# Optimization experiments

Hardware: AMD Instinct MI355X
Metric: run time of the kernel (lower is better)

The kernel has to match this reference:

```python
import jax, jax.numpy as jnp
import numpy as np

EPS = 1e-5

def splice(x, offsets):
    # x: [B, F, T]; offsets already shifted so offsets[0] == 0.
    # Output channel order matches torch reshape(-1, C*F): y[b, f*C+c, t] = x[b, f, t+off[c]]
    w = offsets[-1]
    Tn = x.shape[2] - w
    y = jnp.stack([x[:, :, o:o + Tn] for o in offsets], axis=2)  # [B, F, C, Tn]
    B, F, C, _ = y.shape
    return y.reshape(B, F * C, Tn)

def conv1x1(x, w, b):
    # x: [B, Cin, T], w: [Cout, Cin], b: [Cout]
    return jnp.einsum('oc,bct->bot', w, x) + b[None, :, None]

def bn_ct(x, gamma=None, beta=None):
    # BatchNorm1d (training mode, biased var) over (batch, time) per channel
    m = x.mean(axis=(0, 2), keepdims=True)
    v = x.var(axis=(0, 2), keepdims=True)
    y = (x - m) * jax.lax.rsqrt(v + EPS)
    if gamma is not None:
        y = y * gamma[None, :, None] + beta[None, :, None]
    return y

def bn_c(x, gamma, beta):
    # BatchNorm1d on [B, C]
    m = x.mean(axis=0, keepdims=True)
    v = x.var(axis=0, keepdims=True)
    return (x - m) * jax.lax.rsqrt(v + EPS) * gamma[None, :] + beta[None, :]

def relu6(x):
    return jnp.clip(x, 0.0, 6.0)

def setup_inputs() -> dict:
    key = jax.random.key(0)
    ks = list(jax.random.split(key, 32))
    def rn(shape, scale=0.05):
        return jax.random.normal(ks.pop(), shape, dtype=jnp.float32) * scale
    inp = {
        'x': jax.random.normal(ks.pop(), (32, 2048, 20), dtype=jnp.float32),
        'h1_w': rn((512, 100)), 'h1_b': rn((512,)),
        'h2_w': rn((512, 1536)), 'h2_b': rn((512,)),
        'bn2_g': jnp.ones((512,), jnp.float32), 'bn2_b': jnp.zeros((512,), jnp.float32),
        'h3_w': rn((512, 1536)), 'h3_b': rn((512,)),
        'bn3_g': jnp.ones((512,), jnp.float32), 'bn3_b': jnp.zeros((512,), jnp.float32),
        'h4_w': rn((512, 512)), 'h4_b': rn((512,)),
        'bn4_g': jnp.ones((512,), jnp.float32), 'bn4_b': jnp.zeros((512,), jnp.float32),
        'h5_w': rn((1500, 512)), 'h5_b': rn((1500,)),
        'bn5_g': jnp.ones((1500,), jnp.float32), 'bn5_b': jnp.zeros((1500,), jnp.float32),
        'l1_w': rn((512, 3000)), 'l1_b': rn((512,)),
        'bn6_g': jnp.ones((512,), jnp.float32), 'bn6_b': jnp.zeros((512,), jnp.float32),
        'l2_w': rn((512, 512)), 'l2_b': rn((512,)),
        'bn7_g': jnp.ones((512,), jnp.float32), 'bn7_b': jnp.zeros((512,), jnp.float32),
    }
    return inp

def reference(x, h1_w, h1_b, h2_w, h2_b, bn2_g, bn2_b, h3_w, h3_b, bn3_g, bn3_b,
              h4_w, h4_b, bn4_g, bn4_b, h5_w, h5_b, bn5_g, bn5_b,
              l1_w, l1_b, bn6_g, bn6_b, l2_w, l2_b, bn7_g, bn7_b):
    o = jnp.transpose(x, (0, 2, 1))                     # [B, 20, T]
    o = splice(o, (0, 1, 2, 3, 4))                      # context [-2..2] -> [B, 100, T-4]
    o = bn_ct(jax.nn.relu(conv1x1(o, h1_w, h1_b)))      # bn1 affine=False
    o = splice(o, (0, 2, 4))                            # context [-2,0,2] -> [B, 1536, T-8]
    o = bn_ct(jax.nn.relu(conv1x1(o, h2_w, h2_b)), bn2_g, bn2_b)
    o = splice(o, (0, 3, 6))                            # context [-3,0,3] -> [B, 1536, T-14]
    o = bn_ct(jax.nn.relu(conv1x1(o, h3_w, h3_b)), bn3_g, bn3_b)
    o = bn_ct(relu6(conv1x1(o, h4_w, h4_b)), bn4_g, bn4_b)
    o = bn_ct(relu6(conv1x1(o, h5_w, h5_b)), bn5_g, bn5_b)  # [B, 1500, T']
    mean = o.mean(axis=-1)
    std = jnp.std(o, axis=-1, ddof=1)                   # torch.std is unbiased
    o = jnp.concatenate((mean, std), axis=1)            # [B, 3000]
    o = bn_c(relu6(o @ l1_w.T + l1_b), bn6_g, bn6_b)
    o = bn_c(relu6(o @ l2_w.T + l2_b), bn7_g, bn7_b)
    return o
```

## Files before the change

kernel.cpp:

```cpp
#include <hip/hip_runtime.h>
#include <cstdint>

#define EPSF 1e-5f

namespace {

typedef _Float16 f16;
typedef _Float16 v8h __attribute__((ext_vector_type(8)));
typedef float v4f __attribute__((ext_vector_type(4)));

constexpr int B  = 32;
constexpr int T0 = 2048, F0 = 20;
constexpr int T1 = 2044, T2 = 2040, T3 = 2034;
constexpr int TS = 2048;

__device__ __forceinline__ void gload16(const void* g, void* l) {
    typedef const __attribute__((address_space(1))) void* gp_t;
    typedef __attribute__((address_space(3))) void* lp_t;
    __builtin_amdgcn_global_load_lds((gp_t)(unsigned long long)g,
                                     (lp_t)(unsigned int)(unsigned long long)l,
                                     16, 0, 0);
}
__device__ __forceinline__ void wait_vm4() { asm volatile("s_waitcnt vmcnt(4)" ::: "memory"); }
__device__ __forceinline__ void wait_vm0() { asm volatile("s_waitcnt vmcnt(0)" ::: "memory"); }

__global__ __launch_bounds__(256) void transpose_x(const float* __restrict__ x,
                                                   f16* __restrict__ xT,
                                                   float* __restrict__ stZ)
{
    int idx = blockIdx.x * 256 + threadIdx.x;
    if (idx < 4096) stZ[idx] = 0.f;
    constexpr int total = B * 3 * TS * 8;
    if (idx >= total) return;
    int fl = idx & 7;
    int t  = (idx >> 3) & (TS - 1);
    int fo = (idx >> 14) % 3;
    int b  = idx / (3 << 14);
    int f  = fo * 8 + fl;
    float v = (f < F0) ? x[((size_t)b * T0 + t) * F0 + f] : 0.f;
    xT[idx] = (f16)v;
}

template<int FP, int C>
__global__ __launch_bounds__(256) void fold_mfma(
    const float* __restrict__ W, const float* __restrict__ bias,
    const float* __restrict__ st, const float* __restrict__ gamma, const float* __restrict__ beta,
    f16* __restrict__ Wh, float* __restrict__ bf,
    int Oreal, int Freal, int Cin, int CinOrig, float invN)
{
    int o = blockIdx.x;
    auto sidx = [&](int k) {
        return ((size_t)((o >> 7) * (Cin >> 3) + (k >> 3)) * 128 + (o & 127)) * 8 + (k & 7);
    };
    if (o >= Oreal) {
        for (int k = threadIdx.x; k < Cin; k += 256) Wh[sidx(k)] = (f16)0.f;
        if (threadIdx.x == 0) bf[o] = 0.f;
        return;
    }
    float local = 0.f;
    for (int k = threadIdx.x; k < Cin; k += 256) {
        int c = k / FP, f = k - c * FP;
        float wv = 0.f;
        if (c < C && f < Freal) {
            float sc = 1.f, sh = 0.f;
            if (st) {
                float mean = st[f] * invN;
                float var  = st[Freal + f] * invN - mean * mean;
                sc = rsqrtf(var + EPSF);
                if (gamma) sc *= gamma[f];
                sh = (beta ? beta[f] : 0.f) - mean * sc;
            }
            float w = W[(size_t)o * CinOrig + f * C + c];
            wv = w * sc;
            local += w * sh;
        }
        Wh[sidx(k)] = (f16)wv;
    }
#pragma unroll
    for (int d = 32; d; d >>= 1) local += __shfl_down(local, d);
    __shared__ float red[4];
    if ((threadIdx.x & 63) == 0) red[threadIdx.x >> 6] = local;
    __syncthreads();
    if (threadIdx.x == 0) bf[o] = bias[o] + red[0] + red[1] + red[2] + red[3];
}

template<int ACT, int FPR, int CIN>
__global__ __launch_bounds__(256, 4) void conv_mfma(
    const f16* __restrict__ inT, const f16* __restrict__ Wh,
    const float* __restrict__ bias, f16* __restrict__ outT,
    float* __restrict__ st, int O, int Tout, int offMul)
{
    __shared__ __align__(16) f16 Ilds[2][4 * 128 * 8];
    __shared__ __align__(16) f16 Wlds[2][4 * 128 * 8];
    __shared__ float redS[2][128];
    __shared__ float redQ[2][128];
    const int tid  = threadIdx.x;
    const int lane = tid & 63, wave = tid >> 6;
    const int wt = wave & 1, wo = wave >> 1;
    const int quad = lane >> 4, l16 = lane & 15;
    const int tB = blockIdx.x * 128, oB = blockIdx.y * 128, b = blockIdx.z;
    const f16* inb = inT + (size_t)b * FPR * TS;
    const size_t wBase = (size_t)(oB >> 7) * (CIN >> 3);

    v4f acc[4][4];
#pragma unroll
    for (int mi = 0; mi < 4; ++mi)
#pragma unroll
        for (int ni = 0; ni < 4; ++ni)
#pragma unroll
            for (int r = 0; r < 4; ++r) acc[mi][ni][r] = 0.f;

    constexpr int nIter = CIN >> 5;

    auto compute = [&](int pb) {
        v8h afr[4], bfr[4];
#pragma unroll
        for (int mi = 0; mi < 4; ++mi)
            afr[mi] = *(const v8h*)&Ilds[pb][(quad * 128 + wt * 64 + mi * 16 + l16) * 8];
#pragma unroll
        for (int ni = 0; ni < 4; ++ni)
            bfr[ni] = *(const v8h*)&Wlds[pb][(quad * 128 + wo * 64 + ni * 16 + l16) * 8];
#pragma unroll
        for (int mi = 0; mi < 4; ++mi)
#pragma unroll
            for (int ni = 0; ni < 4; ++ni)
                acc[mi][ni] = __builtin_amdgcn_mfma_f32_16x16x32_f16(
                    afr[mi], bfr[ni], acc[mi][ni], 0, 0, 0);
    };

    if constexpr (FPR == 512) {
        const char* gp0;
        const char* gp1;
        intptr_t dN, dWr;
        if (wave < 2) {
            gp0 = (const char*)(inb + ((size_t)(2 * wave) * TS + tB + lane) * 8);
            gp1 = gp0 + (size_t)TS * 16;
            dN  = (intptr_t)4 * TS * 16;
            dWr = ((intptr_t)(-60) * TS + offMul) * 16;
        } else {
            gp0 = (const char*)(Wh + ((wBase + 2 * (wave - 2)) * 128 + lane) * 8);
            gp1 = gp0;
            dN  = 8192;
            dWr = 8192;
        }
        auto stage_fast = [&](int pb) {
            f16* Ib = &Ilds[pb][0];
            f16* Wb = &Wlds[pb][0];
            if (wave < 2) {
                int k0 = 2 * wave;
                gload16(gp0,        Ib + (k0 * 128) * 8);
                gload16(gp0 + 1024, Ib + (k0 * 128 + 64) * 8);
                gload16(gp1,        Ib + ((k0 + 1) * 128) * 8);
                gload16(gp1 + 1024, Ib + ((k0 + 1) * 128 + 64) * 8);
            } else {
                int k0 = 2 * (wave - 2);
                gload16(gp0,        Wb + (k0 * 128) * 8);
                gload16(gp0 + 1024, Wb + (k0 * 128 + 64) * 8);
                gload16(gp0 + 2048, Wb + ((k0 + 1) * 128) * 8);
                gload16(gp0 + 3072, Wb + ((k0 + 1) * 128 + 64) * 8);
            }
        };
        auto advance = [&](int kFrom) {
            intptr_t d = (((kFrom + 1) & 15) == 0) ? dWr : dN;
            gp0 += d;
            if (wave < 2) gp1 += d;
        };

        stage_fast(0);
        advance(0);
#pragma unroll 2
        for (int k = 0; k < nIter; ++k) {
            const int pb = k & 1;
            __syncthreads();
            if (k + 1 < nIter) { stage_fast(pb ^ 1); advance(k + 1); wait_vm4(); }
            else               { wait_vm0(); }
            __syncthreads();
            compute(pb);
        }
    } else {
        auto stage = [&](int iB, int pb) {
#pragma unroll
            for (int j = 0; j < 4; ++j) {
                int s = wave * 4 + j;
                int koct = (s & 7) >> 1, half = s & 1;
                if (s < 8) {
                    int kidx = iB + koct * 8;
                    int c = kidx / FPR, f = kidx - c * FPR;
                    int t = tB + half * 64 + lane + c * offMul;
                    gload16(inb + ((size_t)(f >> 3) * TS + t) * 8,
                            &Ilds[pb][(koct * 128 + half * 64) * 8]);
                } else {
                    gload16(Wh + ((wBase + (iB >> 3) + koct) * 128 + half * 64 + lane) * 8,
                            &Wlds[pb][(koct * 128 + half * 64) * 8]);
                }
            }
        };
        stage(0, 0);
#pragma unroll 2
        for (int k = 0; k < nIter; ++k) {
            const int pb = k & 1;
            __syncthreads();
            if (k + 1 < nIter) { stage((k + 1) * 32, pb ^ 1); wait_vm4(); }
            else               { wait_vm0(); }
            __syncthreads();
            compute(pb);
        }
    }

    float Sl[4] = {0, 0, 0, 0}, Ql[4] = {0, 0, 0, 0};
#pragma unroll
    for (int ni = 0; ni < 4; ++ni) {
        const int o  = oB + wo * 64 + ni * 16 + l16;
        const float bs = bias[o];
        f16* orow = outT + (size_t)b * O * TS + (size_t)(o >> 3) * TS * 8 + (o & 7);
#pragma unroll
        for (int mi = 0; mi < 4; ++mi)
#pragma unroll
            for (int r = 0; r < 4; ++r) {
                int t = tB + wt * 64 + mi * 16 + quad * 4 + r;
                if (t < Tout) {
                    float v = acc[mi][ni][r] + bs;
                    v = fmaxf(v, 0.f);
                    if (ACT == 2) v = fminf(v, 6.f);
                    orow[(size_t)t * 8] = (f16)v;
                    Sl[ni] += v; Ql[ni] += v * v;
                }
            }
    }
#pragma unroll
    for (int ni = 0; ni < 4; ++ni) {
        float s = Sl[ni], q = Ql[ni];
        s += __shfl_down(s, 32); q += __shfl_down(q, 32);
        s += __shfl_down(s, 16); q += __shfl_down(q, 16);
        if (lane < 16) {
            redS[wt][wo * 64 + ni * 16 + lane] = s;
            redQ[wt][wo * 64 + ni * 16 + lane] = q;
        }
    }
    __syncthreads();
    if (tid < 128) {
        atomicAdd(&st[oB + tid],       redS[0][tid] + redS[1][tid]);
        atomicAdd(&st[512 + oB + tid], redQ[0][tid] + redQ[1][tid]);
    }
}

template<int CIN>
__global__ __launch_bounds__(256, 4) void pool_mfma(
    const f16* __restrict__ inT, const f16* __restrict__ Wh,
    const float* __restrict__ bias, float* __restrict__ Sp, float* __restrict__ Qp,
    int T, int Opad)
{
    const int L    = blockIdx.x;
    const int slot = L >> 3;
    const int oB   = (slot % 12) * 128;
    const int cz   = (L & 7) + 8 * (slot / 12);
    const int b    = cz & 31, z = cz >> 5;

    __shared__ __align__(16) f16 Ilds[2][4 * 128 * 8];
    __shared__ __align__(16) f16 Wlds[2][4 * 128 * 8];
    __shared__ float redS[2][128];
    __shared__ float redQ[2][128];
    const int tid  = threadIdx.x;
    const int lane = tid & 63, wave = tid >> 6;
    const int wt = wave & 1, wo = wave >> 1;
    const int quad = lane >> 4, l16 = lane & 15;
    const f16* inb = inT + (size_t)b * CIN * TS;
    const size_t wBase = (size_t)(oB >> 7) * (CIN >> 3);

    float Sl[4] = {0, 0, 0, 0}, Ql[4] = {0, 0, 0, 0};
    float bs[4];
#pragma unroll
    for (int ni = 0; ni < 4; ++ni) bs[ni] = bias[oB + wo * 64 + ni * 16 + l16];

    const int tBase = z * 512;
    constexpr int kPer  = CIN >> 5;
    constexpr int total = 4 * kPer;

    v4f acc[4][4];
#pragma unroll
    for (int mi = 0; mi < 4; ++mi)
#pragma unroll
        for (int ni = 0; ni < 4; ++ni)
#pragma unroll
            for (int r = 0; r < 4; ++r) acc[mi][ni][r] = 0.f;

    const char* gp0;
    const char* gp1;
    intptr_t dN, dWr;
    if (wave < 2) {
        gp0 = (const char*)(inb + ((size_t)(2 * wave) * TS + tBase + lane) * 8);
        gp1 = gp0 + (size_t)TS * 16;
        dN  = (intptr_t)4 * TS * 16;
        dWr = ((intptr_t)(-60) * TS + 128) * 16;
    } else {
        gp0 = (const char*)(Wh + ((wBase + 2 * (wave - 2)) * 128 + lane) * 8);
        gp1 = gp0;
        dN  = 8192;
        dWr = (intptr_t)(-60) * 128 * 16;
    }
    auto stage_fast = [&](int pb) {
        f16* Ib = &Ilds[pb][0];
        f16* Wb = &Wlds[pb][0];
        if (wave < 2) {
            int k0 = 2 * wave;
            gload16(gp0,        Ib + (k0 * 128) * 8);
            gload16(gp0 + 1024, Ib + (k0 * 128 + 64) * 8);
            gload16(gp1,        Ib + ((k0 + 1) * 128) * 8);
            gload16(gp1 + 1024, Ib + ((k0 + 1) * 128 + 64) * 8);
        } else {
            int k0 = 2 * (wave - 2);
            gload16(gp0,        Wb + (k0 * 128) * 8);
            gload16(gp0 + 1024, Wb + (k0 * 128 + 64) * 8);
            gload16(gp0 + 2048, Wb + ((k0 + 1) * 128) * 8);
            gload16(gp0 + 3072, Wb + ((k0 + 1) * 128 + 64) * 8);
        }
    };
    auto advance = [&](int itFrom) {
        intptr_t d = (((itFrom + 1) & 15) == 0) ? dWr : dN;
        gp0 += d;
        if (wave < 2) gp1 += d;
    };

    stage_fast(0);
    advance(0);
#pragma unroll 2
    for (int it = 0; it < total; ++it) {
        const int pb = it & 1;
        __syncthreads();
        if (it + 1 < total) { stage_fast(pb ^ 1); advance(it + 1); wait_vm4(); }
        else                { wait_vm0(); }
        __syncthreads();
        v8h afr[4], bfr[4];
#pragma unroll
        for (int mi = 0; mi < 4; ++mi)
            afr[mi] = *(const v8h*)&Ilds[pb][(quad * 128 + wt * 64 + mi * 16 + l16) * 8];
#pragma unroll
        for (int ni = 0; ni < 4; ++ni)
            bfr[ni] = *(const v8h*)&Wlds[pb][(quad * 128 + wo * 64 + ni * 16 + l16) * 8];
#pragma unroll
        for (int mi = 0; mi < 4; ++mi)
#pragma unroll
            for (int ni = 0; ni < 4; ++ni)
                acc[mi][ni] = __builtin_amdgcn_mfma_f32_16x16x32_f16(
                    afr[mi], bfr[ni], acc[mi][ni], 0, 0, 0);

        if ((it & (kPer - 1)) == kPer - 1) {
            int tB = tBase + (it >> 4) * 128;
#pragma unroll
            for (int ni = 0; ni < 4; ++ni)
#pragma unroll
                for (int mi = 0; mi < 4; ++mi)
#pragma unroll
                    for (int r = 0; r < 4; ++r) {
                        int t = tB + wt * 64 + mi * 16 + quad * 4 + r;
                        if (t < T) {
                            float v = fminf(fmaxf(acc[mi][ni][r] + bs[ni], 0.f), 6.f);
                            Sl[ni] += v; Ql[ni] += v * v;
                        }
                        acc[mi][ni][r] = 0.f;
                    }
        }
    }

#pragma unroll
    for (int ni = 0; ni < 4; ++ni) {
        float s = Sl[ni], q = Ql[ni];
        s += __shfl_down(s, 32); q += __shfl_down(q, 32);
        s += __shfl_down(s, 16); q += __shfl_down(q, 16);
        if (lane < 16) {
            redS[wt][wo * 64 + ni * 16 + lane] = s;
            redQ[wt][wo * 64 + ni * 16 + lane] = q;
        }
    }
    __syncthreads();
    if (tid < 128) {
        int o = oB + tid;
        Sp[((size_t)z * B + b) * Opad + o] = redS[0][tid] + redS[1][tid];
        Qp[((size_t)z * B + b) * Opad + o] = redQ[0][tid] + redQ[1][tid];
    }
}

__global__ __launch_bounds__(256) void pool_finalize(
    const float* __restrict__ Sp, const float* __restrict__ Qp,
    const float* __restrict__ g5, const float* __restrict__ b5,
    float* __restrict__ stat, int Opad, int Oreal, int T)
{
    int co = blockIdx.x * 256 + threadIdx.x;
    if (co >= Oreal) return;
    double sS = 0, sQ = 0;
    for (int z = 0; z < 4; ++z)
        for (int b = 0; b < B; ++b) {
            sS += Sp[((size_t)z * B + b) * Opad + co];
            sQ += Qp[((size_t)z * B + b) * Opad + co];
        }
    double invN = 1.0 / ((double)B * T);
    double m = sS * invN;
    double v = sQ * invN - m * m;
    float sc = g5[co] * rsqrtf((float)v + EPSF);
    float sh = b5[co] - (float)m * sc;
    for (int b = 0; b < B; ++b) {
        double sb = 0, qb = 0;
        for (int z = 0; z < 4; ++z) {
            sb += Sp[((size_t)z * B + b) * Opad + co];
            qb += Qp[((size_t)z * B + b) * Opad + co];
        }
        double mb = sb / T;
        double vb = (qb - sb * sb / T) / (T - 1);
        if (vb < 0) vb = 0;
        stat[(size_t)b * 2 * Oreal + co]         = (float)mb * sc + sh;
        stat[(size_t)b * 2 * Oreal + Oreal + co] = sqrtf((float)vb) * fabsf(sc);
    }
}

__global__ __launch_bounds__(256) void fc_relu6(const float* __restrict__ x,
                                                const float* __restrict__ W,
                                                const float* __restrict__ bias,
                                                float* __restrict__ y, int Cin, int O)
{
    int wid = (blockIdx.x * 256 + threadIdx.x) >> 6;
    int lane = threadIdx.x & 63;
    if (wid >= B * O) return;
    int b = wid / O, o = wid - b * O;
    const float* xr = x + (size_t)b * Cin;
    const float* wr = W + (size_t)o * Cin;
    float s = 0.f;
    for (int c = lane; c < Cin; c += 64) s = fmaf(xr[c], wr[c], s);
#pragma unroll
    for (int d = 32; d; d >>= 1) s += __shfl_down(s, d);
    if (lane == 0) y[wid] = fminf(fmaxf(s + bias[o], 0.f), 6.f);
}

__global__ __launch_bounds__(512) void bn_batch(const float* __restrict__ x,
                                                const float* __restrict__ g,
                                                const float* __restrict__ be,
                                                float* __restrict__ y, int O)
{
    int o = threadIdx.x;
    if (o >= O) return;
    float s = 0.f, q = 0.f;
    for (int b = 0; b < B; ++b) { float v = x[b * O + o]; s += v; q += v * v; }
    float m = s / B;
    float var = q / B - m * m;
    float sc = g[o] * rsqrtf(var + EPSF);
    float sh = be[o] - m * sc;
    for (int b = 0; b < B; ++b) y[b * O + o] = x[b * O + o] * sc + sh;
}

}

extern "C" void kernel_launch(void* const* d_in, const int* in_sizes, int n_in,
                              void* d_out, int out_size, void* d_ws, size_t ws_size,
                              hipStream_t stream)
{
    (void)in_sizes; (void)n_in; (void)out_size; (void)ws_size;
    const float* x     = (const float*)d_in[0];
    const float* h1_w  = (const float*)d_in[1];
    const float* h1_b  = (const float*)d_in[2];
    const float* h2_w  = (const float*)d_in[3];
    const float* h2_b  = (const float*)d_in[4];
    const float* bn2_g = (const float*)d_in[5];
    const float* bn2_b = (const float*)d_in[6];
    const float* h3_w  = (const float*)d_in[7];
    const float* h3_b  = (const float*)d_in[8];
    const float* bn3_g = (const float*)d_in[9];
    const float* bn3_b = (const float*)d_in[10];
    const float* h4_w  = (const float*)d_in[11];
    const float* h4_b  = (const float*)d_in[12];
    const float* bn4_g = (const float*)d_in[13];
    const float* bn4_b = (const float*)d_in[14];
    const float* h5_w  = (const float*)d_in[15];
    const float* h5_b  = (const float*)d_in[16];
    const float* bn5_g = (const float*)d_in[17];
    const float* bn5_b = (const float*)d_in[18];
    const float* l1_w  = (const float*)d_in[19];
    const float* l1_b  = (const float*)d_in[20];
    const float* bn6_g = (const float*)d_in[21];
    const float* bn6_b = (const float*)d_in[22];
    const float* l2_w  = (const float*)d_in[23];
    const float* l2_b  = (const float*)d_in[24];
    const float* bn7_g = (const float*)d_in[25];
    const float* bn7_b = (const float*)d_in[26];

    char* ws = (char*)d_ws;
    size_t off = 0;
    auto alloc = [&](size_t bytes) {
        char* p = ws + off;
        off += (bytes + 255) & ~(size_t)255;
        return (void*)p;
    };
    f16* xT    = (f16*)alloc(((size_t)B * 3  * TS * 8 + 2048) * 2);
    f16* bufA  = (f16*)alloc(((size_t)B * 64 * TS * 8 + 2048) * 2);
    f16* bufB  = (f16*)alloc(((size_t)B * 64 * TS * 8 + 2048) * 2);
    f16* Wh1   = (f16*)alloc((size_t)512 * 128 * 2);
    f16* Wh2   = (f16*)alloc((size_t)512 * 1536 * 2);
    f16* Wh3   = (f16*)alloc((size_t)512 * 1536 * 2);
    f16* Wh4   = (f16*)alloc((size_t)512 * 512 * 2);
    f16* Wh5   = (f16*)alloc((size_t)1536 * 512 * 2);
    float* bf1 = (float*)alloc(512 * 4);
    float* bf2 = (float*)alloc(512 * 4);
    float* bf3 = (float*)alloc(512 * 4);
    float* bf4 = (float*)alloc(512 * 4);
    float* bf5 = (float*)alloc(1536 * 4);
    float* stZ = (float*)alloc(4096 * 4);
    float* st1 = stZ, *st2 = stZ + 1024, *st3 = stZ + 2048, *st4 = stZ + 3072;
    float* Sp  = (float*)alloc((size_t)4 * B * 1536 * 4);
    float* Qp  = (float*)alloc((size_t)4 * B * 1536 * 4);
    float* stat = (float*)alloc((size_t)B * 3000 * 4);
    float* f1  = (float*)alloc((size_t)B * 512 * 4);
    float* f2  = (float*)alloc((size_t)B * 512 * 4);

    transpose_x<<<(B * 3 * TS * 8 + 255) / 256, 256, 0, stream>>>(x, xT, stZ);

    fold_mfma<24, 5><<<512, 256, 0, stream>>>(h1_w, h1_b, nullptr, nullptr, nullptr,
                                              Wh1, bf1, 512, 20, 128, 100, 0.f);
    conv_mfma<1, 24, 128><<<dim3(16, 4, B), 256, 0, stream>>>(
        xT, Wh1, bf1, bufA, st1, 512, T1, 1);

    fold_mfma<512, 3><<<512, 256, 0, stream>>>(h2_w, h2_b, st1, nullptr, nullptr,
                                               Wh2, bf2, 512, 512, 1536, 1536,
                                               1.f / (B * T1));
    conv_mfma<1, 512, 1536><<<dim3(16, 4, B), 256, 0, stream>>>(
        bufA, Wh2, bf2, bufB, st2, 512, T2, 2);

    fold_mfma<512, 3><<<512, 256, 0, stream>>>(h3_w, h3_b, st2, bn2_g, bn2_b,
                                               Wh3, bf3, 512, 512, 1536, 1536,
                                               1.f / (B * T2));
    conv_mfma<1, 512, 1536><<<dim3(16, 4, B), 256, 0, stream>>>(
        bufB, Wh3, bf3, bufA, st3, 512, T3, 3);

    fold_mfma<512, 1><<<512, 256, 0, stream>>>(h4_w, h4_b, st3, bn3_g, bn3_b,
                                               Wh4, bf4, 512, 512, 512, 512,
                                               1.f / (B * T3));
    conv_mfma<2, 512, 512><<<dim3(16, 4, B), 256, 0, stream>>>(
        bufA, Wh4, bf4, bufB, st4, 512, T3, 0);

    fold_mfma<512, 1><<<1536, 256, 0, stream>>>(h5_w, h5_b, st4, bn4_g, bn4_b,
                                                Wh5, bf5, 1500, 512, 512, 512,
                                                1.f / (B * T3));
    pool_mfma<512><<<1536, 256, 0, stream>>>(bufB, Wh5, bf5, Sp, Qp, T3, 1536);

    pool_finalize<<<6, 256, 0, stream>>>(Sp, Qp, bn5_g, bn5_b, stat, 1536, 1500, T3);

    fc_relu6<<<(B * 512 * 64 + 255) / 256, 256, 0, stream>>>(stat, l1_w, l1_b, f1, 3000, 512);
    bn_batch<<<1, 512, 0, stream>>>(f1, bn6_g, bn6_b, f1, 512);
    fc_relu6<<<(B * 512 * 64 + 255) / 256, 256, 0, stream>>>(f1, l2_w, l2_b, f2, 512, 512);
    bn_batch<<<1, 512, 0, stream>>>(f2, bn7_g, bn7_b, (float*)d_out, 512);
}
```

Before: 660.1 us.

## Replace conv and pool GEMMs with 256x256-tile 8-wave pipelined MFMA kernel

Adds a conv8p kernel that uses 512 threads and a 256x256 output tile with 64-deep K steps. The operand loads are interleaved with quarter-tile MFMA groups, using raw s_barrier, setprio and vmcnt waits for finer-grained overlap. Layers 2 to 5, including the pooled layer 5, now go through this kernel, and the pool partial count rises from 4 to 8 time chunks. The larger tiles aim to raise arithmetic intensity and hide load latency, at the cost of more registers and LDS (two blocks per CU). The old conv_mfma fast path for FPR==512 is removed, so the generic path remains only for layer 1.

```diff
diff --git a/kernel.cpp b/kernel.cpp
--- a/kernel.cpp
+++ b/kernel.cpp
@@ -21,8 +21,11 @@
                                      (lp_t)(unsigned int)(unsigned long long)l,
                                      16, 0, 0);
 }
+__device__ __forceinline__ void wait_vm6() { asm volatile("s_waitcnt vmcnt(6)" ::: "memory"); }
 __device__ __forceinline__ void wait_vm4() { asm volatile("s_waitcnt vmcnt(4)" ::: "memory"); }
 __device__ __forceinline__ void wait_vm0() { asm volatile("s_waitcnt vmcnt(0)" ::: "memory"); }
+
+#define BARRIER asm volatile("s_barrier" ::: "memory")
 
 __global__ __launch_bounds__(256) void transpose_x(const float* __restrict__ x,
                                                    f16* __restrict__ xT,
@@ -128,83 +131,32 @@
                     afr[mi], bfr[ni], acc[mi][ni], 0, 0, 0);
     };
 
-    if constexpr (FPR == 512) {
-        const char* gp0;
-        const char* gp1;
-        intptr_t dN, dWr;
-        if (wave < 2) {
-            gp0 = (const char*)(inb + ((size_t)(2 * wave) * TS + tB + lane) * 8);
-            gp1 = gp0 + (size_t)TS * 16;
-            dN  = (intptr_t)4 * TS * 16;
-            dWr = ((intptr_t)(-60) * TS + offMul) * 16;
-        } else {
-            gp0 = (const char*)(Wh + ((wBase + 2 * (wave - 2)) * 128 + lane) * 8);
-            gp1 = gp0;
-            dN  = 8192;
-            dWr = 8192;
-        }
-        auto stage_fast = [&](int pb) {
-            f16* Ib = &Ilds[pb][0];
-            f16* Wb = &Wlds[pb][0];
-            if (wave < 2) {
-                int k0 = 2 * wave;
-                gload16(gp0,        Ib + (k0 * 128) * 8);
-                gload16(gp0 + 1024, Ib + (k0 * 128 + 64) * 8);
-                gload16(gp1,        Ib + ((k0 + 1) * 128) * 8);
-                gload16(gp1 + 1024, Ib + ((k0 + 1) * 128 + 64) * 8);
+    auto stage = [&](int iB, int pb) {
+#pragma unroll
+        for (int j = 0; j < 4; ++j) {
+            int s = wave * 4 + j;
+            int koct = (s & 7) >> 1, half = s & 1;
+            if (s < 8) {
+                int kidx = iB + koct * 8;
+                int c = kidx / FPR, f = kidx - c * FPR;
+                int t = tB + half * 64 + lane + c * offMul;
+                gload16(inb + ((size_t)(f >> 3) * TS + t) * 8,
+                        &Ilds[pb][(koct * 128 + half * 64) * 8]);
             } else {
-                int k0 = 2 * (wave - 2);
-                gload16(gp0,        Wb + (k0 * 128) * 8);
-                gload16(gp0 + 1024, Wb + (k0 * 128 + 64) * 8);
-                gload16(gp0 + 2048, Wb + ((k0 + 1) * 128) * 8);
-                gload16(gp0 + 3072, Wb + ((k0 + 1) * 128 + 64) * 8);
+                gload16(Wh + ((wBase + (iB >> 3) + koct) * 128 + half * 64 + lane) * 8,
+                        &Wlds[pb][(koct * 128 + half * 64) * 8]);
             }
-        };
-        auto advance = [&](int kFrom) {
-            intptr_t d = (((kFrom + 1) & 15) == 0) ? dWr : dN;
-            gp0 += d;
-            if (wave < 2) gp1 += d;
-        };
-
-        stage_fast(0);
-        advance(0);
+        }
+    };
+    stage(0, 0);
 #pragma unroll 2
-        for (int k = 0; k < nIter; ++k) {
-            const int pb = k & 1;
-            __syncthreads();
-            if (k + 1 < nIter) { stage_fast(pb ^ 1); advance(k + 1); wait_vm4(); }
-            else               { wait_vm0(); }
-            __syncthreads();
-            compute(pb);
-        }
-    } else {
-        auto stage = [&](int iB, int pb) {
-#pragma unroll
-            for (int j = 0; j < 4; ++j) {
-                int s = wave * 4 + j;
-                int koct = (s & 7) >> 1, half = s & 1;
-                if (s < 8) {
-                    int kidx = iB + koct * 8;
-                    int c = kidx / FPR, f = kidx - c * FPR;
-                    int t = tB + half * 64 + lane + c * offMul;
-                    gload16(inb + ((size_t)(f >> 3) * TS + t) * 8,
-                            &Ilds[pb][(koct * 128 + half * 64) * 8]);
-                } else {
-                    gload16(Wh + ((wBase + (iB >> 3) + koct) * 128 + half * 64 + lane) * 8,
-                            &Wlds[pb][(koct * 128 + half * 64) * 8]);
-                }
-            }
-        };
-        stage(0, 0);
-#pragma unroll 2
-        for (int k = 0; k < nIter; ++k) {
-            const int pb = k & 1;
-            __syncthreads();
-            if (k + 1 < nIter) { stage((k + 1) * 32, pb ^ 1); wait_vm4(); }
-            else               { wait_vm0(); }
-            __syncthreads();
-            compute(pb);
-        }
+    for (int k = 0; k < nIter; ++k) {
+        const int pb = k & 1;
+        __syncthreads();
+        if (k + 1 < nIter) { stage((k + 1) * 32, pb ^ 1); wait_vm4(); }
+        else               { wait_vm0(); }
+        __syncthreads();
+        compute(pb);
     }
 
     float Sl[4] = {0, 0, 0, 0}, Ql[4] = {0, 0, 0, 0};
@@ -244,139 +196,203 @@
     }
 }
 
-template<int CIN>
-__global__ __launch_bounds__(256, 4) void pool_mfma(
+
+#define LDSB_M(PB, NH) do {                                                          \
+    _Pragma("unroll")                                                                \
+    for (int n2 = 0; n2 < 2; ++n2) {                                                 \
+        _Pragma("unroll")                                                            \
+        for (int ks = 0; ks < 2; ++ks)                                               \
+            bfr[NH][n2][ks] = *(const v8h*)&Wlds[PB][((ks * 4 + quad) * 256 +        \
+                (NH) * 128 + wo * 32 + n2 * 16 + l16) * 8];                          \
+    }                                                                                \
+} while (0)
+
+#define MFMA_Q(MH, NH) do {                                                          \
+    asm volatile("s_waitcnt lgkmcnt(0)" ::: "memory");                               \
+    __builtin_amdgcn_sched_barrier(0);                                               \
+    __builtin_amdgcn_s_setprio(1);                                                   \
+    _Pragma("unroll")                                                                \
+    for (int m4 = 0; m4 < 4; ++m4) {                                                 \
+        _Pragma("unroll")                                                            \
+        for (int n2 = 0; n2 < 2; ++n2) {                                             \
+            _Pragma("unroll")                                                        \
+            for (int ks = 0; ks < 2; ++ks)                                           \
+                acc[(MH) * 4 + m4][(NH) * 2 + n2] =                                  \
+                    __builtin_amdgcn_mfma_f32_16x16x32_f16(                          \
+                        afr[m4][ks], bfr[NH][n2][ks],                                \
+                        acc[(MH) * 4 + m4][(NH) * 2 + n2], 0, 0, 0);                 \
+        }                                                                            \
+    }                                                                                \
+    __builtin_amdgcn_s_setprio(0);                                                   \
+} while (0)
+
+template<int ACT, int CIN, bool POOL>
+__global__ __launch_bounds__(512, 2) void conv8p(
     const f16* __restrict__ inT, const f16* __restrict__ Wh,
-    const float* __restrict__ bias, float* __restrict__ Sp, float* __restrict__ Qp,
-    int T, int Opad)
-{
-    const int L    = blockIdx.x;
-    const int slot = L >> 3;
-    const int oB   = (slot % 12) * 128;
-    const int cz   = (L & 7) + 8 * (slot / 12);
-    const int b    = cz & 31, z = cz >> 5;
-
-    __shared__ __align__(16) f16 Ilds[2][4 * 128 * 8];
-    __shared__ __align__(16) f16 Wlds[2][4 * 128 * 8];
-    __shared__ float redS[2][128];
-    __shared__ float redQ[2][128];
-    const int tid  = threadIdx.x;
+    const float* __restrict__ bias, f16* __restrict__ outT,
+    float* __restrict__ st, float* __restrict__ Sp, float* __restrict__ Qp,
+    int O, int Tout, int offMul, int Opad)
+{
+    constexpr bool SPLICE = (CIN == 1536);
+    constexpr int NT = CIN / 64;
+    constexpr int nIter = NT / 2;
+    __shared__ __align__(16) f16 Ilds[2][8 * 256 * 8];
+    __shared__ __align__(16) f16 Wlds[2][8 * 256 * 8];
+    __shared__ float redS[8][64];
+    __shared__ float redQ[8][64];
+
+    const int tid = threadIdx.x;
     const int lane = tid & 63, wave = tid >> 6;
     const int wt = wave & 1, wo = wave >> 1;
     const int quad = lane >> 4, l16 = lane & 15;
-    const f16* inb = inT + (size_t)b * CIN * TS;
-    const size_t wBase = (size_t)(oB >> 7) * (CIN >> 3);
+    const int tB = blockIdx.x * 256, oB = blockIdx.y * 256, b = blockIdx.z;
+    const f16* inb = inT + (size_t)b * 64 * TS * 8;
+    const int sBase = oB >> 7;
+    const int octSel = tid >> 7;
+    const int tPos = tid & 127;
+
+    auto stageA = [&](int pb, int kt, int mh) {
+#pragma unroll
+        for (int cc = 0; cc < 2; ++cc) {
+            const int octL = cc * 4 + octSel;
+            const int octG = kt * 8 + octL;
+            const int t = tB + mh * 128 + tPos;
+            const f16* src;
+            if constexpr (SPLICE) {
+                const int cx = octG >> 6;
+                const int fo = octG & 63;
+                src = inb + ((size_t)fo * TS + t + cx * offMul) * 8;
+            } else {
+                src = inb + ((size_t)octG * TS + t) * 8;
+            }
+            gload16(src, &Ilds[pb][(octL * 256 + mh * 128 + tPos) * 8]);
+        }
+    };
+    auto stageB = [&](int pb, int kt, int nh) {
+#pragma unroll
+        for (int cc = 0; cc < 2; ++cc) {
+            const int octL = cc * 4 + octSel;
+            const f16* src = Wh + (((size_t)(sBase + nh) * (CIN >> 3) + kt * 8 + octL) * 128 + tPos) * 8;
+            gload16(src, &Wlds[pb][(octL * 256 + nh * 128 + tPos) * 8]);
+        }
+    };
+
+    v4f acc[8][4];
+#pragma unroll
+    for (int m = 0; m < 8; ++m)
+#pragma unroll
+        for (int n = 0; n < 4; ++n)
+#pragma unroll
+            for (int r = 0; r < 4; ++r) acc[m][n][r] = 0.f;
+
+    v8h afr[4][2];
+    v8h bfr[2][2][2];
+
+    auto ldsA = [&](int pb, int mh) {
+#pragma unroll
+        for (int m4 = 0; m4 < 4; ++m4)
+#pragma unroll
+            for (int ks = 0; ks < 2; ++ks)
+                afr[m4][ks] = *(const v8h*)&Ilds[pb][((ks * 4 + quad) * 256 +
+                    mh * 128 + wt * 64 + m4 * 16 + l16) * 8];
+    };
+
+    stageA(0, 0, 0); stageB(0, 0, 0);
+    stageB(0, 0, 1); stageA(0, 0, 1);
+    stageA(1, 1, 0); stageB(1, 1, 0); stageB(1, 1, 1);
+    wait_vm6();
+    BARRIER;
+
+#pragma unroll 1
+    for (int i = 0; i < nIter; ++i) {
+        const int kt1 = 2 * i + 1;
+        const int kn0 = 2 * i + 2, kn1 = 2 * i + 3;
+        const bool more = (i + 1 < nIter);
+        ldsA(0, 0); LDSB_M(0, 0);
+        stageA(1, kt1, 1);
+        BARRIER;
+        MFMA_Q(0, 0);
+        BARRIER;
+        LDSB_M(0, 1);
+        if (more) stageA(0, kn0, 0);
+        BARRIER;
+        MFMA_Q(0, 1);
+        BARRIER;
+        ldsA(0, 1);
+        if (more) stageB(0, kn0, 0);
+        BARRIER;
+        MFMA_Q(1, 0);
+        BARRIER;
+        if (more) { stageB(0, kn0, 1); wait_vm6(); } else wait_vm0();
+        BARRIER;
+        MFMA_Q(1, 1);
+        BARRIER;
+        ldsA(1, 0); LDSB_M(1, 0);
+        if (more) stageA(0, kn0, 1);
+        BARRIER;
+        MFMA_Q(0, 0);
+        BARRIER;
+        LDSB_M(1, 1);
+        if (more) stageA(1, kn1, 0);
+        BARRIER;
+        MFMA_Q(0, 1);
+        BARRIER;
+        ldsA(1, 1);
+        if (more) stageB(1, kn1, 0);
+        BARRIER;
+        MFMA_Q(1, 0);
+        BARRIER;
+        if (more) { stageB(1, kn1, 1); wait_vm6(); }
+        BARRIER;
+        MFMA_Q(1, 1);
+        BARRIER;
+    }
 
     float Sl[4] = {0, 0, 0, 0}, Ql[4] = {0, 0, 0, 0};
-    float bs[4];
-#pragma unroll
-    for (int ni = 0; ni < 4; ++ni) bs[ni] = bias[oB + wo * 64 + ni * 16 + l16];
-
-    const int tBase = z * 512;
-    constexpr int kPer  = CIN >> 5;
-    constexpr int total = 4 * kPer;
-
-    v4f acc[4][4];
-#pragma unroll
-    for (int mi = 0; mi < 4; ++mi)
-#pragma unroll
-        for (int ni = 0; ni < 4; ++ni)
-#pragma unroll
-            for (int r = 0; r < 4; ++r) acc[mi][ni][r] = 0.f;
-
-    const char* gp0;
-    const char* gp1;
-    intptr_t dN, dWr;
-    if (wave < 2) {
-        gp0 = (const char*)(inb + ((size_t)(2 * wave) * TS + tBase + lane) * 8);
-        gp1 = gp0 + (size_t)TS * 16;
-        dN  = (intptr_t)4 * TS * 16;
-        dWr = ((intptr_t)(-60) * TS + 128) * 16;
-    } else {
-        gp0 = (const char*)(Wh + ((wBase + 2 * (wave - 2)) * 128 + lane) * 8);
-        gp1 = gp0;
-        dN  = 8192;
-        dWr = (intptr_t)(-60) * 128 * 16;
-    }
-    auto stage_fast = [&](int pb) {
-        f16* Ib = &Ilds[pb][0];
-        f16* Wb = &Wlds[pb][0];
-        if (wave < 2) {
-            int k0 = 2 * wave;
-            gload16(gp0,        Ib + (k0 * 128) * 8);
-            gload16(gp0 + 1024, Ib + (k0 * 128 + 64) * 8);
-            gload16(gp1,        Ib + ((k0 + 1) * 128) * 8);
-            gload16(gp1 + 1024, Ib + ((k0 + 1) * 128 + 64) * 8);
-        } else {
-            int k0 = 2 * (wave - 2);
-            gload16(gp0,        Wb + (k0 * 128) * 8);
-            gload16(gp0 + 1024, Wb + (k0 * 128 + 64) * 8);
-            gload16(gp0 + 2048, Wb + ((k0 + 1) * 128) * 8);
-            gload16(gp0 + 3072, Wb + ((k0 + 1) * 128 + 64) * 8);
-        }
-    };
-    auto advance = [&](int itFrom) {
-        intptr_t d = (((itFrom + 1) & 15) == 0) ? dWr : dN;
-        gp0 += d;
-        if (wave < 2) gp1 += d;
-    };
-
-    stage_fast(0);
-    advance(0);
-#pragma unroll 2
-    for (int it = 0; it < total; ++it) {
-        const int pb = it & 1;
-        __syncthreads();
-        if (it + 1 < total) { stage_fast(pb ^ 1); advance(it + 1); wait_vm4(); }
-        else                { wait_vm0(); }
-        __syncthreads();
-        v8h afr[4], bfr[4];
-#pragma unroll
-        for (int mi = 0; mi < 4; ++mi)
-            afr[mi] = *(const v8h*)&Ilds[pb][(quad * 128 + wt * 64 + mi * 16 + l16) * 8];
-#pragma unroll
-        for (int ni = 0; ni < 4; ++ni)
-            bfr[ni] = *(const v8h*)&Wlds[pb][(quad * 128 + wo * 64 + ni * 16 + l16) * 8];
-#pragma unroll
-        for (int mi = 0; mi < 4; ++mi)
-#pragma unroll
-            for (int ni = 0; ni < 4; ++ni)
-                acc[mi][ni] = __builtin_amdgcn_mfma_f32_16x16x32_f16(
-                    afr[mi], bfr[ni], acc[mi][ni], 0, 0, 0);
-
-        if ((it & (kPer - 1)) == kPer - 1) {
-            int tB = tBase + (it >> 4) * 128;
-#pragma unroll
-            for (int ni = 0; ni < 4; ++ni)
-#pragma unroll
-                for (int mi = 0; mi < 4; ++mi)
-#pragma unroll
-                    for (int r = 0; r < 4; ++r) {
-                        int t = tB + wt * 64 + mi * 16 + quad * 4 + r;
-                        if (t < T) {
-                            float v = fminf(fmaxf(acc[mi][ni][r] + bs[ni], 0.f), 6.f);
-                            Sl[ni] += v; Ql[ni] += v * v;
-                        }
-                        acc[mi][ni][r] = 0.f;
-                    }
-        }
-    }
-
-#pragma unroll
-    for (int ni = 0; ni < 4; ++ni) {
-        float s = Sl[ni], q = Ql[ni];
+#pragma unroll
+    for (int n = 0; n < 4; ++n) {
+        const int oLoc = (n >> 1) * 128 + wo * 32 + (n & 1) * 16 + l16;
+        const int o = oB + oLoc;
+        const float bs = bias[o];
+        f16* orow = nullptr;
+        if constexpr (!POOL)
+            orow = outT + (size_t)b * O * TS + (size_t)(o >> 3) * TS * 8 + (o & 7);
+#pragma unroll
+        for (int m = 0; m < 8; ++m)
+#pragma unroll
+            for (int r = 0; r < 4; ++r) {
+                const int t = tB + (m >> 2) * 128 + wt * 64 + (m & 3) * 16 + quad * 4 + r;
+                if (t < Tout) {
+                    float v = acc[m][n][r] + bs;
+                    v = fmaxf(v, 0.f);
+                    if (ACT == 2) v = fminf(v, 6.f);
+                    if constexpr (!POOL) orow[(size_t)t * 8] = (f16)v;
+                    Sl[n] += v; Ql[n] += v * v;
+                }
+            }
+    }
+#pragma unroll
+    for (int n = 0; n < 4; ++n) {
+        float s = Sl[n], q = Ql[n];
         s += __shfl_down(s, 32); q += __shfl_down(q, 32);
         s += __shfl_down(s, 16); q += __shfl_down(q, 16);
-        if (lane < 16) {
-            redS[wt][wo * 64 + ni * 16 + lane] = s;
-            redQ[wt][wo * 64 + ni * 16 + lane] = q;
-        }
+        if (lane < 16) { redS[wave][n * 16 + lane] = s; redQ[wave][n * 16 + lane] = q; }
     }
     __syncthreads();
-    if (tid < 128) {
-        int o = oB + tid;
-        Sp[((size_t)z * B + b) * Opad + o] = redS[0][tid] + redS[1][tid];
-        Qp[((size_t)z * B + b) * Opad + o] = redQ[0][tid] + redQ[1][tid];
+    if (tid < 256) {
+        const int rem = tid & 127;
+        const int wo2 = rem >> 5;
+        const int nn  = (tid >> 7) * 2 + ((rem >> 4) & 1);
+        const int l   = tid & 15;
+        const float s = redS[wo2 * 2][nn * 16 + l] + redS[wo2 * 2 + 1][nn * 16 + l];
+        const float q = redQ[wo2 * 2][nn * 16 + l] + redQ[wo2 * 2 + 1][nn * 16 + l];
+        if constexpr (POOL) {
+            Sp[((size_t)blockIdx.x * B + b) * Opad + oB + tid] = s;
+            Qp[((size_t)blockIdx.x * B + b) * Opad + oB + tid] = q;
+        } else {
+            atomicAdd(&st[oB + tid], s);
+            atomicAdd(&st[512 + oB + tid], q);
+        }
     }
 }
 
@@ -388,7 +404,7 @@
     int co = blockIdx.x * 256 + threadIdx.x;
     if (co >= Oreal) return;
     double sS = 0, sQ = 0;
-    for (int z = 0; z < 4; ++z)
+    for (int z = 0; z < 8; ++z)
         for (int b = 0; b < B; ++b) {
             sS += Sp[((size_t)z * B + b) * Opad + co];
             sQ += Qp[((size_t)z * B + b) * Opad + co];
@@ -400,7 +416,7 @@
     float sh = b5[co] - (float)m * sc;
     for (int b = 0; b < B; ++b) {
         double sb = 0, qb = 0;
-        for (int z = 0; z < 4; ++z) {
+        for (int z = 0; z < 8; ++z) {
             sb += Sp[((size_t)z * B + b) * Opad + co];
             qb += Qp[((size_t)z * B + b) * Opad + co];
         }
@@ -503,8 +519,8 @@
     float* bf5 = (float*)alloc(1536 * 4);
     float* stZ = (float*)alloc(4096 * 4);
     float* st1 = stZ, *st2 = stZ + 1024, *st3 = stZ + 2048, *st4 = stZ + 3072;
-    float* Sp  = (float*)alloc((size_t)4 * B * 1536 * 4);
-    float* Qp  = (float*)alloc((size_t)4 * B * 1536 * 4);
+    float* Sp  = (float*)alloc((size_t)8 * B * 1536 * 4);
+    float* Qp  = (float*)alloc((size_t)8 * B * 1536 * 4);
     float* stat = (float*)alloc((size_t)B * 3000 * 4);
     float* f1  = (float*)alloc((size_t)B * 512 * 4);
     float* f2  = (float*)alloc((size_t)B * 512 * 4);
@@ -519,25 +535,26 @@
     fold_mfma<512, 3><<<512, 256, 0, stream>>>(h2_w, h2_b, st1, nullptr, nullptr,
                                                Wh2, bf2, 512, 512, 1536, 1536,
                                                1.f / (B * T1));
-    conv_mfma<1, 512, 1536><<<dim3(16, 4, B), 256, 0, stream>>>(
-        bufA, Wh2, bf2, bufB, st2, 512, T2, 2);
+    conv8p<1, 1536, false><<<dim3(8, 2, B), 512, 0, stream>>>(
+        bufA, Wh2, bf2, bufB, st2, nullptr, nullptr, 512, T2, 2, 0);
 
     fold_mfma<512, 3><<<512, 256, 0, stream>>>(h3_w, h3_b, st2, bn2_g, bn2_b,
                                                Wh3, bf3, 512, 512, 1536, 1536,
                                                1.f / (B * T2));
-    conv_mfma<1, 512, 1536><<<dim3(16, 4, B), 256, 0, stream>>>(
-        bufB, Wh3, bf3, bufA, st3, 512, T3, 3);
+    conv8p<1, 1536, false><<<dim3(8, 2, B), 512, 0, stream>>>(
+        bufB, Wh3, bf3, bufA, st3, nullptr, nullptr, 512, T3, 3, 0);
 
     fold_mfma<512, 1><<<512, 256, 0, stream>>>(h4_w, h4_b, st3, bn3_g, bn3_b,
                                                Wh4, bf4, 512, 512, 512, 512,
                                                1.f / (B * T3));
-    conv_mfma<2, 512, 512><<<dim3(16, 4, B), 256, 0, stream>>>(
-        bufA, Wh4, bf4, bufB, st4, 512, T3, 0);
+    conv8p<2, 512, false><<<dim3(8, 2, B), 512, 0, stream>>>(
+        bufA, Wh4, bf4, bufB, st4, nullptr, nullptr, 512, T3, 0, 0);
 
     fold_mfma<512, 1><<<1536, 256, 0, stream>>>(h5_w, h5_b, st4, bn4_g, bn4_b,
                                                 Wh5, bf5, 1500, 512, 512, 512,
                                                 1.f / (B * T3));
-    pool_mfma<512><<<1536, 256, 0, stream>>>(bufB, Wh5, bf5, Sp, Qp, T3, 1536);
+    conv8p<2, 512, true><<<dim3(8, 6, B), 512, 0, stream>>>(
+        bufB, Wh5, bf5, nullptr, nullptr, Sp, Qp, 1536, T3, 0, 1536);
 
     pool_finalize<<<6, 256, 0, stream>>>(Sp, Qp, bn5_g, bn5_b, stat, 1536, 1500, T3);
 
```

After: 676.4 us. +2.5%, slower.
